# Optimization experiments

Measured on AMD Instinct MI355X. Metric: run time of the kernel, lower is better.

## Reference

```python
import jax, jax.numpy as jnp
import numpy as np

B, L, F, H = 4096, 32, 28, 512  # batch, max CDR length (=input_size), features, hidden


def setup_inputs() -> dict:
    key = jax.random.key(0)
    ks = jax.random.split(key, 8)
    return {
        "input": jax.random.normal(ks[0], (B, L, F), jnp.float32),
        "unpacked_masks": jnp.ones((B, L, 1), jnp.float32),
        "bias_mat": jnp.zeros((B, L, F), jnp.float32),
        "conv1_w": jax.random.normal(ks[1], (F, F, 3), jnp.float32) * 0.1,
        "conv1_b": jnp.zeros((F,), jnp.float32),
        "conv_w": jax.random.normal(ks[2], (1, L, 1), jnp.float32) * 0.1,
        "conv_b": jnp.zeros((1,), jnp.float32),
        "fc1_w": jax.random.normal(ks[3], (1, H), jnp.float32) * 0.05,
        "fc1_b": jnp.zeros((1,), jnp.float32),
        "W_ih": jax.random.normal(ks[4], (4 * H, L), jnp.float32) * 0.1,
        "W_hh": jax.random.normal(ks[5], (4 * H, H), jnp.float32) * 0.05,
        "b_ih": jnp.zeros((4 * H,), jnp.float32),
        "b_hh": jnp.zeros((4 * H,), jnp.float32),
        "conv2_w": jax.random.normal(ks[6], (1, H, 1), jnp.float32) * 0.05,
        "conv2_b": jnp.zeros((1,), jnp.float32),
    }


def reference(input, unpacked_masks, bias_mat, conv1_w, conv1_b, conv_w, conv_b,
              fc1_w, fc1_b, W_ih, W_hh, b_ih, b_hh, conv2_w, conv2_b):
    b, l, f = input.shape
    h_dim = W_hh.shape[1]
    # --- conv1 residual block (eval mode: dropouts are identity) ---
    x_t = jnp.transpose(input, (0, 2, 1))  # [B, F, L]
    y = jax.lax.conv_general_dilated(
        x_t, conv1_w, window_strides=(1,), padding=[(1, 1)],
        dimension_numbers=("NCH", "OIH", "NCH")) + conv1_b[None, :, None]
    x = jnp.transpose(y, (0, 2, 1)) * unpacked_masks  # [B, L, F]
    x = jax.nn.elu(x) + input
    # --- u_a = Conv1d(L,1,1) over the length axis: [B, 1, F] (kept as [B, F]) ---
    u_a = jnp.einsum("blf,l->bf", x, conv_w[0, :, 0]) + conv_b  # [B, F]
    x_transposed = jnp.transpose(x, (0, 2, 1))  # [B, F, L]

    h0 = jnp.zeros((l, h_dim), input.dtype)
    c0 = jnp.zeros((l, h_dim), input.dtype)

    def step(carry, inps):
        h, c = carry
        u_b, xT_b, bias_b = inps  # [F], [F, L], [L, F]
        w_a = h @ fc1_w.T + fc1_b  # [L, 1]
        scores = jax.nn.leaky_relu(u_b[None, :] + w_a, 0.01) + bias_b  # [L, F]
        attn = jax.nn.softmax(scores, axis=0)  # softmax over dim 1 of [B, L, F]
        ctx = attn @ xT_b  # [L, F] @ [F, L] -> [L, L]
        gates = ctx @ W_ih.T + b_ih + h @ W_hh.T + b_hh  # [L, 4H]
        i_g, f_g, g_g, o_g = jnp.split(gates, 4, axis=-1)
        c_new = jax.nn.sigmoid(f_g) * c + jax.nn.sigmoid(i_g) * jnp.tanh(g_g)
        h_new = jax.nn.sigmoid(o_g) * jnp.tanh(c_new)
        return (h_new, c_new), h_new

    # The original loops over the batch dim, carrying (h, c) across iterations.
    (_, _), all_hidden = jax.lax.scan(step, (h0, c0), (u_a, x_transposed, bias_mat))
    # all_hidden: [B, L, H]
    out = jnp.einsum("blh,h->bl", all_hidden, conv2_w[0, :, 0])[..., None] + conv2_b  # [B, L, 1]
    return out * unpacked_masks
```

## Files before the change

kernel.cpp:

```cpp
#include <hip/hip_runtime.h>
#include <math.h>

#define NBATCH 4096
#define LSEQ   32
#define FDIM   28
#define HDIM   512
#define GBLK   64
#define HSTRIDE 548
#define XSTR    36

typedef int   i32x4 __attribute__((ext_vector_type(4)));
typedef float f32x4 __attribute__((ext_vector_type(4)));
typedef short short8 __attribute__((ext_vector_type(8)));

#define OFF_X    0u
#define OFF_UA   (OFF_X  + 4096u*896u)
#define OFF_BG   (OFF_UA + 4096u*28u)
#define OFF_H    (OFF_BG + 2048u)
#define OFF_BAR  (OFF_H  + 2u*32u*512u)
#define OFF_WFH  (OFF_BAR + 64u)
#define OFF_WFL  (OFF_WFH + 557056u)

__device__ __forceinline__ unsigned bfr(float x) {
    unsigned u = __builtin_bit_cast(unsigned, x);
    return (u + 0x7FFFu + ((u >> 16) & 1u)) >> 16;
}
__device__ __forceinline__ float fb(unsigned b) { return __builtin_bit_cast(float, b << 16); }
__device__ __forceinline__ unsigned packhl(float v) {
    unsigned h = bfr(v);
    unsigned l = bfr(v - fb(h));
    return h | (l << 16);
}
__device__ __forceinline__ float up(unsigned u) {
    return __builtin_bit_cast(float, u << 16) + __builtin_bit_cast(float, u & 0xFFFF0000u);
}
__device__ __forceinline__ float sigm(float v) { return 1.0f / (1.0f + __expf(-v)); }

__global__ __launch_bounds__(256) void prep_kernel(
    const float* __restrict__ input, const float* __restrict__ masks,
    const float* __restrict__ c1w, const float* __restrict__ c1b,
    const float* __restrict__ convw, const float* __restrict__ convb,
    float* __restrict__ xout, float* __restrict__ uaout)
{
    __shared__ float in_lds[32][28];
    __shared__ float w_lds[28][28][3];
    __shared__ float xo[32][28];
    __shared__ float m_lds[32];
    __shared__ float cb_lds[28];
    const int b = blockIdx.x, tid = threadIdx.x;

    for (int i = tid; i < 896; i += 256) in_lds[i / 28][i % 28] = input[(size_t)b * 896 + i];
    for (int i = tid; i < 2352; i += 256) {
        int o = i / 84, r = i % 84;
        w_lds[o][r / 3][r % 3] = c1w[i];
    }
    if (tid < 32) m_lds[tid] = masks[b * 32 + tid];
    if (tid < 28) cb_lds[tid] = c1b[tid];
    __syncthreads();

    for (int i = tid; i < 896; i += 256) {
        const int l = i / 28, f = i % 28;
        float acc = cb_lds[f];
        for (int ii = 0; ii < 28; ++ii) {
            if (l > 0)  acc = fmaf(in_lds[l - 1][ii], w_lds[f][ii][0], acc);
            acc = fmaf(in_lds[l][ii], w_lds[f][ii][1], acc);
            if (l < 31) acc = fmaf(in_lds[l + 1][ii], w_lds[f][ii][2], acc);
        }
        float v = acc * m_lds[l];
        v = (v > 0.f) ? v : expm1f(v);
        v += in_lds[l][f];
        xo[l][f] = v;
        xout[(size_t)b * 896 + i] = v;
    }
    __syncthreads();
    if (tid < 28) {
        float s = convb[0];
        for (int l = 0; l < 32; ++l) s = fmaf(xo[l][tid], convw[l], s);
        uaout[b * 28 + tid] = s;
    }
}

__global__ __launch_bounds__(256) void prepw_kernel(
    const float* __restrict__ bih, const float* __restrict__ bhh, float* __restrict__ BG)
{
    const int g = blockIdx.x * 256 + threadIdx.x;
    BG[g] = bih[g] + bhh[g];
}

__global__ __launch_bounds__(256) void prepf_kernel(
    const float* __restrict__ Wih, const float* __restrict__ Whh,
    unsigned* __restrict__ wfh, unsigned* __restrict__ wfl)
{
    const int id = blockIdx.x * 256 + threadIdx.x;
    const int lane = id & 63;
    int rest = id >> 6;
    const int ct = rest & 1; rest >>= 1;
    const int t = rest % 17, blk = rest / 17;
    const int n = lane & 15, kg = lane >> 4;
    const int c = ct * 16 + n;
    const int g = (c >> 3) * 512 + blk * 8 + (c & 7);
    const int kbase = t * 32 + kg * 8;
    i32x4 hv, lv;
    #pragma unroll
    for (int d = 0; d < 4; ++d) {
        const int k = kbase + 2 * d;
        float w0 = (k     < 512) ? Whh[(size_t)g * 512 + k]     : Wih[g * 32 + (k - 512)];
        float w1 = (k + 1 < 512) ? Whh[(size_t)g * 512 + k + 1] : Wih[g * 32 + (k + 1 - 512)];
        unsigned h0 = bfr(w0), h1 = bfr(w1);
        unsigned l0 = bfr(w0 - fb(h0)), l1 = bfr(w1 - fb(h1));
        ((unsigned*)&hv)[d] = h0 | (h1 << 16);
        ((unsigned*)&lv)[d] = l0 | (l1 << 16);
    }
    ((i32x4*)wfh)[id] = hv;
    ((i32x4*)wfl)[id] = lv;
}

__device__ __forceinline__ void stage_h16(const unsigned* hsrc, unsigned* h_lds, int tid)
{
    const int half = tid >> 7, t128 = tid & 127;
    const unsigned* p = hsrc + half * 8192 + t128 * 4;
    i32x4 v0, v1, v2, v3, v4, v5, v6, v7, v8, v9, v10, v11, v12, v13, v14, v15;
    asm volatile(
        "global_load_dwordx4 %0, %16, off sc0 sc1\n\t"
        "global_load_dwordx4 %1, %16, off offset:2048 sc0 sc1\n\t"
        "global_load_dwordx4 %2, %17, off sc0 sc1\n\t"
        "global_load_dwordx4 %3, %17, off offset:2048 sc0 sc1\n\t"
        "global_load_dwordx4 %4, %18, off sc0 sc1\n\t"
        "global_load_dwordx4 %5, %18, off offset:2048 sc0 sc1\n\t"
        "global_load_dwordx4 %6, %19, off sc0 sc1\n\t"
        "global_load_dwordx4 %7, %19, off offset:2048 sc0 sc1\n\t"
        "global_load_dwordx4 %8, %20, off sc0 sc1\n\t"
        "global_load_dwordx4 %9, %20, off offset:2048 sc0 sc1\n\t"
        "global_load_dwordx4 %10, %21, off sc0 sc1\n\t"
        "global_load_dwordx4 %11, %21, off offset:2048 sc0 sc1\n\t"
        "global_load_dwordx4 %12, %22, off sc0 sc1\n\t"
        "global_load_dwordx4 %13, %22, off offset:2048 sc0 sc1\n\t"
        "global_load_dwordx4 %14, %23, off sc0 sc1\n\t"
        "global_load_dwordx4 %15, %23, off offset:2048 sc0 sc1\n\t"
        "s_waitcnt vmcnt(0)"
        : "=&v"(v0), "=&v"(v1), "=&v"(v2), "=&v"(v3),
          "=&v"(v4), "=&v"(v5), "=&v"(v6), "=&v"(v7),
          "=&v"(v8), "=&v"(v9), "=&v"(v10), "=&v"(v11),
          "=&v"(v12), "=&v"(v13), "=&v"(v14), "=&v"(v15)
        : "v"(p), "v"(p + 1024), "v"(p + 2048), "v"(p + 3072),
          "v"(p + 4096), "v"(p + 5120), "v"(p + 6144), "v"(p + 7168)
        : "memory");
    const int col = t128 * 4;
    const int rb = half * 16;
    *(i32x4*)&h_lds[(rb +  0) * HSTRIDE + col] = v0;
    *(i32x4*)&h_lds[(rb +  1) * HSTRIDE + col] = v1;
    *(i32x4*)&h_lds[(rb +  2) * HSTRIDE + col] = v2;
    *(i32x4*)&h_lds[(rb +  3) * HSTRIDE + col] = v3;
    *(i32x4*)&h_lds[(rb +  4) * HSTRIDE + col] = v4;
    *(i32x4*)&h_lds[(rb +  5) * HSTRIDE + col] = v5;
    *(i32x4*)&h_lds[(rb +  6) * HSTRIDE + col] = v6;
    *(i32x4*)&h_lds[(rb +  7) * HSTRIDE + col] = v7;
    *(i32x4*)&h_lds[(rb +  8) * HSTRIDE + col] = v8;
    *(i32x4*)&h_lds[(rb +  9) * HSTRIDE + col] = v9;
    *(i32x4*)&h_lds[(rb + 10) * HSTRIDE + col] = v10;
    *(i32x4*)&h_lds[(rb + 11) * HSTRIDE + col] = v11;
    *(i32x4*)&h_lds[(rb + 12) * HSTRIDE + col] = v12;
    *(i32x4*)&h_lds[(rb + 13) * HSTRIDE + col] = v13;
    *(i32x4*)&h_lds[(rb + 14) * HSTRIDE + col] = v14;
    *(i32x4*)&h_lds[(rb + 15) * HSTRIDE + col] = v15;
}

__device__ __forceinline__ void build_frag(const unsigned* base, short8& hi, short8& lo)
{
    i32x4 ua = *(const i32x4*)base;
    i32x4 ub = *(const i32x4*)(base + 4);
    i32x4 h, l;
    h.x = (int)__builtin_amdgcn_perm((unsigned)ua.y, (unsigned)ua.x, 0x05040100u);
    l.x = (int)__builtin_amdgcn_perm((unsigned)ua.y, (unsigned)ua.x, 0x07060302u);
    h.y = (int)__builtin_amdgcn_perm((unsigned)ua.w, (unsigned)ua.z, 0x05040100u);
    l.y = (int)__builtin_amdgcn_perm((unsigned)ua.w, (unsigned)ua.z, 0x07060302u);
    h.z = (int)__builtin_amdgcn_perm((unsigned)ub.y, (unsigned)ub.x, 0x05040100u);
    l.z = (int)__builtin_amdgcn_perm((unsigned)ub.y, (unsigned)ub.x, 0x07060302u);
    h.w = (int)__builtin_amdgcn_perm((unsigned)ub.w, (unsigned)ub.z, 0x05040100u);
    l.w = (int)__builtin_amdgcn_perm((unsigned)ub.w, (unsigned)ub.z, 0x07060302u);
    hi = __builtin_bit_cast(short8, h);
    lo = __builtin_bit_cast(short8, l);
}

__device__ __forceinline__ float exact_gate(const unsigned* hrow,
    const float* __restrict__ Whh, const float* __restrict__ Wih, int g)
{
    const f32x4* wr = (const f32x4*)(Whh + (size_t)g * 512);
    float s = 0.f;
    #pragma unroll 4
    for (int q = 0; q < 128; ++q) {
        f32x4 w = wr[q];
        s += up(hrow[4 * q + 0]) * w.x + up(hrow[4 * q + 1]) * w.y
           + up(hrow[4 * q + 2]) * w.z + up(hrow[4 * q + 3]) * w.w;
    }
    const float* wi = Wih + g * 32;
    #pragma unroll 8
    for (int j = 0; j < 32; ++j) s += up(hrow[512 + j]) * wi[j];
    return s;
}

__device__ __forceinline__ void out_proj(const unsigned* h_lds, const float* c2w_lds, float c2b,
                                         const float* masks, float* out, int bb,
                                         int slot16, int seg16)
{
    float p0 = 0.f, p1 = 0.f;
    #pragma unroll
    for (int jj = 0; jj < 8; ++jj) {
        const int off = seg16 * 4 + 64 * jj;
        f32x4 w = *(const f32x4*)&c2w_lds[off];
        i32x4 h0 = *(const i32x4*)&h_lds[slot16 * HSTRIDE + off];
        i32x4 h1 = *(const i32x4*)&h_lds[(slot16 + 16) * HSTRIDE + off];
        p0 += up((unsigned)h0.x) * w.x + up((unsigned)h0.y) * w.y
            + up((unsigned)h0.z) * w.z + up((unsigned)h0.w) * w.w;
        p1 += up((unsigned)h1.x) * w.x + up((unsigned)h1.y) * w.y
            + up((unsigned)h1.z) * w.z + up((unsigned)h1.w) * w.w;
    }
    p0 += __shfl_xor(p0, 1); p0 += __shfl_xor(p0, 2);
    p0 += __shfl_xor(p0, 4); p0 += __shfl_xor(p0, 8);
    p1 += __shfl_xor(p1, 1); p1 += __shfl_xor(p1, 2);
    p1 += __shfl_xor(p1, 4); p1 += __shfl_xor(p1, 8);
    if (seg16 == 0) {
        out[bb * 32 + slot16]      = (p0 + c2b) * masks[bb * 32 + slot16];
        out[bb * 32 + slot16 + 16] = (p1 + c2b) * masks[bb * 32 + slot16 + 16];
    }
}

__global__ __launch_bounds__(256, 1) void rnn_serial(
    const float* __restrict__ xbuf, const float* __restrict__ uabuf,
    const float* __restrict__ BG,
    const unsigned* __restrict__ wfh, const unsigned* __restrict__ wfl,
    const float* __restrict__ Whh, const float* __restrict__ Wih,
    unsigned* hbuf, int* bar,
    const float* __restrict__ bias_mat, const float* __restrict__ masks,
    const float* __restrict__ fc1w, const float* __restrict__ fc1bp,
    const float* __restrict__ c2w, const float* __restrict__ c2bp,
    float* __restrict__ out)
{
    __shared__ unsigned h_lds[32 * HSTRIDE];
    __shared__ float x_lds[32 * XSTR];
    __shared__ float bias_lds[32 * XSTR];
    __shared__ float attn_lds[32 * XSTR];
    __shared__ float gl_part[4 * 32 * 33];
    __shared__ float wapart[4][2][32];
    __shared__ float wa_lds[32];
    __shared__ float ua_lds[28];
    __shared__ float fc1_lds[512];
    __shared__ float c2w_lds[512];
    __shared__ int   s_flag;

    const int tid  = threadIdx.x;
    const int blk  = blockIdx.x;
    const int lane = tid & 63;
    const int wv   = tid >> 6;

    for (int i = tid; i < 512; i += 256) { fc1_lds[i] = fc1w[i]; c2w_lds[i] = c2w[i]; }
    if (tid == 0) s_flag = 0;
    const float f1b = fc1bp[0];
    const float c2b = c2bp[0];

    i32x4 whi[4][2], wlo[4][2];
    {
        const i32x4* wfh4 = (const i32x4*)wfh;
        const i32x4* wfl4 = (const i32x4*)wfl;
        #pragma unroll
        for (int s = 0; s < 4; ++s)
            #pragma unroll
            for (int ct = 0; ct < 2; ++ct) {
                const int idx = ((blk * 17 + wv * 4 + s) * 2 + ct) * 64 + lane;
                whi[s][ct] = wfh4[idx];
                wlo[s][ct] = wfl4[idx];
            }
    }
    i32x4 w16h[2], w16l[2];
    if (wv == 0) {
        const i32x4* wfh4 = (const i32x4*)wfh;
        const i32x4* wfl4 = (const i32x4*)wfl;
        #pragma unroll
        for (int ct = 0; ct < 2; ++ct) {
            const int idx = ((blk * 17 + 16) * 2 + ct) * 64 + lane;
            w16h[ct] = wfh4[idx];
            w16l[ct] = wfl4[idx];
        }
    }
    i32x4 wAh[4], wAl[4];
    {
        const int n = lane & 15, kg = lane >> 4;
        #pragma unroll
        for (int s = 0; s < 4; ++s) {
            wAh[s] = (i32x4){0, 0, 0, 0};
            wAl[s] = (i32x4){0, 0, 0, 0};
            if (n < 2) {
                const float* src = (n == 0) ? fc1w : c2w;
                const int k0 = (wv * 4 + s) * 32 + kg * 8;
                #pragma unroll
                for (int d = 0; d < 4; ++d) {
                    float v0 = src[k0 + 2 * d], v1 = src[k0 + 2 * d + 1];
                    unsigned h0 = bfr(v0), h1 = bfr(v1);
                    unsigned l0 = bfr(v0 - fb(h0)), l1 = bfr(v1 - fb(h1));
                    ((unsigned*)&wAh[s])[d] = h0 | (h1 << 16);
                    ((unsigned*)&wAl[s])[d] = l0 | (l1 << 16);
                }
            }
        }
    }

    const int l_own = tid >> 3, hc = tid & 7;
    float bgv[4];
    #pragma unroll
    for (int t = 0; t < 4; ++t) bgv[t] = BG[t * 512 + blk * 8 + hc];
    float c_reg = 0.f;
    bool use_mfma = true;

    float4 xr = make_float4(0.f, 0.f, 0.f, 0.f), br = xr;
    float ua_r = 0.f;
    if (tid < 224) {
        xr = *(const float4*)(xbuf + tid * 4);
        br = *(const float4*)(bias_mat + tid * 4);
    }
    if (tid < 28) ua_r = uabuf[tid];

    const int slot16 = tid >> 4, seg16 = tid & 15;
    const int arow = lane & 15, kg = lane >> 4;
    __syncthreads();

    for (int b = 0; b < NBATCH; ++b) {
        stage_h16(hbuf + (b & 1) * 16384, h_lds, tid);
        if (tid < 224) {
            #pragma unroll
            for (int i = 0; i < 4; ++i) {
                const int idx = tid * 4 + i;
                const int l = idx / 28, f = idx - l * 28;
                x_lds[l * XSTR + f]    = ((const float*)&xr)[i];
                bias_lds[l * XSTR + f] = ((const float*)&br)[i];
            }
        }
        if (tid < 28) ua_lds[tid] = ua_r;
        __syncthreads();

        f32x4 accg[2][2], accw[2];
        if (use_mfma) {
            accg[0][0] = (f32x4){0,0,0,0}; accg[0][1] = (f32x4){0,0,0,0};
            accg[1][0] = (f32x4){0,0,0,0}; accg[1][1] = (f32x4){0,0,0,0};
            accw[0]    = (f32x4){0,0,0,0}; accw[1]    = (f32x4){0,0,0,0};
            #pragma unroll
            for (int s = 0; s < 4; ++s) {
                const int k0 = (wv * 4 + s) * 32 + kg * 8;
                short8 ah0, al0, ah1, al1;
                build_frag(&h_lds[arow * HSTRIDE + k0], ah0, al0);
                build_frag(&h_lds[(arow + 16) * HSTRIDE + k0], ah1, al1);
                #pragma unroll
                for (int ct = 0; ct < 2; ++ct) {
                    short8 bh = __builtin_bit_cast(short8, whi[s][ct]);
                    short8 bl = __builtin_bit_cast(short8, wlo[s][ct]);
                    accg[ct][0] = __builtin_amdgcn_mfma_f32_16x16x32_bf16(ah0, bh, accg[ct][0], 0, 0, 0);
                    accg[ct][0] = __builtin_amdgcn_mfma_f32_16x16x32_bf16(al0, bh, accg[ct][0], 0, 0, 0);
                    accg[ct][0] = __builtin_amdgcn_mfma_f32_16x16x32_bf16(ah0, bl, accg[ct][0], 0, 0, 0);
                    accg[ct][1] = __builtin_amdgcn_mfma_f32_16x16x32_bf16(ah1, bh, accg[ct][1], 0, 0, 0);
                    accg[ct][1] = __builtin_amdgcn_mfma_f32_16x16x32_bf16(al1, bh, accg[ct][1], 0, 0, 0);
                    accg[ct][1] = __builtin_amdgcn_mfma_f32_16x16x32_bf16(ah1, bl, accg[ct][1], 0, 0, 0);
                }
                short8 bh = __builtin_bit_cast(short8, wAh[s]);
                short8 bl = __builtin_bit_cast(short8, wAl[s]);
                accw[0] = __builtin_amdgcn_mfma_f32_16x16x32_bf16(ah0, bh, accw[0], 0, 0, 0);
                accw[0] = __builtin_amdgcn_mfma_f32_16x16x32_bf16(al0, bh, accw[0], 0, 0, 0);
                accw[0] = __builtin_amdgcn_mfma_f32_16x16x32_bf16(ah0, bl, accw[0], 0, 0, 0);
                accw[1] = __builtin_amdgcn_mfma_f32_16x16x32_bf16(ah1, bh, accw[1], 0, 0, 0);
                accw[1] = __builtin_amdgcn_mfma_f32_16x16x32_bf16(al1, bh, accw[1], 0, 0, 0);
                accw[1] = __builtin_amdgcn_mfma_f32_16x16x32_bf16(ah1, bl, accw[1], 0, 0, 0);
            }
            if (wv != 0) {
                #pragma unroll
                for (int ct = 0; ct < 2; ++ct)
                    #pragma unroll
                    for (int rt = 0; rt < 2; ++rt)
                        #pragma unroll
                        for (int r = 0; r < 4; ++r)
                            gl_part[(wv * 32 + rt * 16 + kg * 4 + r) * 33 + ct * 16 + (lane & 15)] = accg[ct][rt][r];
            }
            const int n = lane & 15;
            if (n < 2) {
                #pragma unroll
                for (int rt = 0; rt < 2; ++rt)
                    #pragma unroll
                    for (int r = 0; r < 4; ++r)
                        wapart[wv][n][rt * 16 + kg * 4 + r] = accw[rt][r];
            }
        }
        if (b < 2 || !use_mfma) {
            float p0 = 0.f, p1 = 0.f;
            #pragma unroll
            for (int jj = 0; jj < 8; ++jj) {
                const int off = seg16 * 4 + 64 * jj;
                f32x4 w = *(const f32x4*)&fc1_lds[off];
                i32x4 h0 = *(const i32x4*)&h_lds[slot16 * HSTRIDE + off];
                i32x4 h1 = *(const i32x4*)&h_lds[(slot16 + 16) * HSTRIDE + off];
                p0 += up((unsigned)h0.x) * w.x + up((unsigned)h0.y) * w.y
                    + up((unsigned)h0.z) * w.z + up((unsigned)h0.w) * w.w;
                p1 += up((unsigned)h1.x) * w.x + up((unsigned)h1.y) * w.y
                    + up((unsigned)h1.z) * w.z + up((unsigned)h1.w) * w.w;
            }
            p0 += __shfl_xor(p0, 1); p0 += __shfl_xor(p0, 2);
            p0 += __shfl_xor(p0, 4); p0 += __shfl_xor(p0, 8);
            p1 += __shfl_xor(p1, 1); p1 += __shfl_xor(p1, 2);
            p1 += __shfl_xor(p1, 4); p1 += __shfl_xor(p1, 8);
            if (seg16 == 0) { wa_lds[slot16] = p0 + f1b; wa_lds[slot16 + 16] = p1 + f1b; }
            if (b > 0 && blk == ((b - 1) & 63))
                out_proj(h_lds, c2w_lds, c2b, masks, out, b - 1, slot16, seg16);
        }
        __syncthreads();

        if (wv == 3) {
            if (use_mfma && lane < 32) {
                float wm = f1b;
                #pragma unroll
                for (int w = 0; w < 4; ++w) wm += wapart[w][0][lane];
                if (b < 2) {
                    if (fabsf(wm - wa_lds[lane]) > 0.02f + 0.004f * fabsf(wa_lds[lane])) s_flag = 1;
                } else {
                    wa_lds[lane] = wm;
                }
            }
            if (lane < 56) {
                const int f = lane >> 1, hf = lane & 1;
                const float uaf = ua_lds[f];
                float z[16], mx = -1e30f;
                #pragma unroll
                for (int i = 0; i < 16; ++i) {
                    const int l = hf * 16 + i;
                    float v = uaf + wa_lds[l];
                    v = (v >= 0.f) ? v : 0.01f * v;
                    v += bias_lds[l * XSTR + f];
                    z[i] = v;
                    mx = fmaxf(mx, v);
                }
                mx = fmaxf(mx, __shfl_xor(mx, 1));
                float sum = 0.f;
                #pragma unroll
                for (int i = 0; i < 16; ++i) { z[i] = __expf(z[i] - mx); sum += z[i]; }
                sum += __shfl_xor(sum, 1);
                const float inv = 1.0f / sum;
                #pragma unroll
                for (int i = 0; i < 16; ++i) attn_lds[(hf * 16 + i) * XSTR + f] = z[i] * inv;
            }
        } else if (wv == 2 && use_mfma && lane < 32) {
            float om = c2b;
            #pragma unroll
            for (int w = 0; w < 4; ++w) om += wapart[w][1][lane];
            if (b < 2) {
                const unsigned* hr = &h_lds[lane * HSTRIDE];
                float ox = c2b;
                for (int k = 0; k < 512; ++k) ox += up(hr[k]) * c2w_lds[k];
                if (fabsf(om - ox) > 0.02f + 0.004f * fabsf(ox)) s_flag = 1;
            } else if (b > 0 && blk == ((b - 1) & 63)) {
                out[(b - 1) * 32 + lane] = om * masks[(b - 1) * 32 + lane];
            }
        }
        __syncthreads();

        {
            const int j0 = hc * 4;
            float t0v = 0.f, t1v = 0.f, t2v = 0.f, t3v = 0.f;
            #pragma unroll
            for (int fo = 0; fo < 7; ++fo) {
                f32x4 a4 = *(const f32x4*)&attn_lds[l_own * XSTR + fo * 4];
                f32x4 x0 = *(const f32x4*)&x_lds[(j0 + 0) * XSTR + fo * 4];
                f32x4 x1 = *(const f32x4*)&x_lds[(j0 + 1) * XSTR + fo * 4];
                f32x4 x2 = *(const f32x4*)&x_lds[(j0 + 2) * XSTR + fo * 4];
                f32x4 x3 = *(const f32x4*)&x_lds[(j0 + 3) * XSTR + fo * 4];
                t0v += a4.x * x0.x + a4.y * x0.y + a4.z * x0.z + a4.w * x0.w;
                t1v += a4.x * x1.x + a4.y * x1.y + a4.z * x1.z + a4.w * x1.w;
                t2v += a4.x * x2.x + a4.y * x2.y + a4.z * x2.z + a4.w * x2.w;
                t3v += a4.x * x3.x + a4.y * x3.y + a4.z * x3.z + a4.w * x3.w;
            }
            i32x4 cp;
            cp.x = (int)packhl(t0v); cp.y = (int)packhl(t1v);
            cp.z = (int)packhl(t2v); cp.w = (int)packhl(t3v);
            *(i32x4*)&h_lds[l_own * HSTRIDE + 512 + j0] = cp;
        }
        {
            const int bn = (b + 1 < NBATCH) ? b + 1 : 0;
            if (tid < 224) {
                xr = *(const float4*)(xbuf + (size_t)bn * 896 + tid * 4);
                br = *(const float4*)(bias_mat + (size_t)bn * 896 + tid * 4);
            }
            if (tid < 28) ua_r = uabuf[bn * 28 + tid];
        }
        __syncthreads();

        if (use_mfma && wv == 0) {
            short8 ah0, al0, ah1, al1;
            build_frag(&h_lds[arow * HSTRIDE + 512 + kg * 8], ah0, al0);
            build_frag(&h_lds[(arow + 16) * HSTRIDE + 512 + kg * 8], ah1, al1);
            #pragma unroll
            for (int ct = 0; ct < 2; ++ct) {
                short8 bh = __builtin_bit_cast(short8, w16h[ct]);
                short8 bl = __builtin_bit_cast(short8, w16l[ct]);
                accg[ct][0] = __builtin_amdgcn_mfma_f32_16x16x32_bf16(ah0, bh, accg[ct][0], 0, 0, 0);
                accg[ct][0] = __builtin_amdgcn_mfma_f32_16x16x32_bf16(al0, bh, accg[ct][0], 0, 0, 0);
                accg[ct][0] = __builtin_amdgcn_mfma_f32_16x16x32_bf16(ah0, bl, accg[ct][0], 0, 0, 0);
                accg[ct][1] = __builtin_amdgcn_mfma_f32_16x16x32_bf16(ah1, bh, accg[ct][1], 0, 0, 0);
                accg[ct][1] = __builtin_amdgcn_mfma_f32_16x16x32_bf16(al1, bh, accg[ct][1], 0, 0, 0);
                accg[ct][1] = __builtin_amdgcn_mfma_f32_16x16x32_bf16(ah1, bl, accg[ct][1], 0, 0, 0);
            }
            #pragma unroll
            for (int ct = 0; ct < 2; ++ct)
                #pragma unroll
                for (int rt = 0; rt < 2; ++rt)
                    #pragma unroll
                    for (int r = 0; r < 4; ++r)
                        gl_part[(rt * 16 + kg * 4 + r) * 33 + ct * 16 + (lane & 15)] = accg[ct][rt][r];
        }
        __syncthreads();

        {
            float gv[4];
            #pragma unroll
            for (int t = 0; t < 4; ++t) {
                float g = bgv[t];
                if (use_mfma) {
                    #pragma unroll
                    for (int w = 0; w < 4; ++w)
                        g += gl_part[(w * 32 + l_own) * 33 + t * 8 + hc];
                }
                gv[t] = g;
            }
            if (b < 2) {
                bool bad = false;
                #pragma unroll
                for (int t = 0; t < 4; ++t) {
                    float ref = bgv[t] + exact_gate(&h_lds[l_own * HSTRIDE], Whh, Wih,
                                                    t * 512 + blk * 8 + hc);
                    if (use_mfma && fabsf(gv[t] - ref) > 0.02f + 0.004f * fabsf(ref)) bad = true;
                    gv[t] = ref;
                }
                if (bad) s_flag = 1;
                __syncthreads();
                use_mfma = use_mfma && (s_flag == 0);
                __syncthreads();
                if (tid == 0) s_flag = 0;
            } else if (!use_mfma) {
                #pragma unroll
                for (int t = 0; t < 4; ++t)
                    gv[t] = bgv[t] + exact_gate(&h_lds[l_own * HSTRIDE], Whh, Wih,
                                                t * 512 + blk * 8 + hc);
            }
            const float cn = sigm(gv[1]) * c_reg + sigm(gv[0]) * tanhf(gv[2]);
            const float hn = sigm(gv[3]) * tanhf(cn);
            c_reg = cn;
            __hip_atomic_store(hbuf + ((b & 1) ^ 1) * 16384 + l_own * 512 + blk * 8 + hc,
                               packhl(hn), __ATOMIC_RELAXED, __HIP_MEMORY_SCOPE_AGENT);
        }
        asm volatile("s_waitcnt vmcnt(0)" ::: "memory");
        __syncthreads();
        if (tid == 0)
            __hip_atomic_store(&bar[blk], b + 1, __ATOMIC_RELAXED, __HIP_MEMORY_SCOPE_AGENT);
        if (tid < 64) {
            while (true) {
                int v = __hip_atomic_load(&bar[tid], __ATOMIC_RELAXED, __HIP_MEMORY_SCOPE_AGENT);
                if (__all(v >= b + 1)) break;
                __builtin_amdgcn_s_sleep(1);
            }
        }
        __syncthreads();
    }

    if (blk == 63) {
        stage_h16(hbuf, h_lds, tid);
        __syncthreads();
        if (use_mfma) {
            f32x4 accw[2];
            accw[0] = (f32x4){0,0,0,0}; accw[1] = (f32x4){0,0,0,0};
            #pragma unroll
            for (int s = 0; s < 4; ++s) {
                const int k0 = (wv * 4 + s) * 32 + kg * 8;
                short8 ah0, al0, ah1, al1;
                build_frag(&h_lds[arow * HSTRIDE + k0], ah0, al0);
                build_frag(&h_lds[(arow + 16) * HSTRIDE + k0], ah1, al1);
                short8 bh = __builtin_bit_cast(short8, wAh[s]);
                short8 bl = __builtin_bit_cast(short8, wAl[s]);
                accw[0] = __builtin_amdgcn_mfma_f32_16x16x32_bf16(ah0, bh, accw[0], 0, 0, 0);
                accw[0] = __builtin_amdgcn_mfma_f32_16x16x32_bf16(al0, bh, accw[0], 0, 0, 0);
                accw[0] = __builtin_amdgcn_mfma_f32_16x16x32_bf16(ah0, bl, accw[0], 0, 0, 0);
                accw[1] = __builtin_amdgcn_mfma_f32_16x16x32_bf16(ah1, bh, accw[1], 0, 0, 0);
                accw[1] = __builtin_amdgcn_mfma_f32_16x16x32_bf16(al1, bh, accw[1], 0, 0, 0);
                accw[1] = __builtin_amdgcn_mfma_f32_16x16x32_bf16(ah1, bl, accw[1], 0, 0, 0);
            }
            const int n = lane & 15;
            if (n < 2) {
                #pragma unroll
                for (int rt = 0; rt < 2; ++rt)
                    #pragma unroll
                    for (int r = 0; r < 4; ++r)
                        wapart[wv][n][rt * 16 + kg * 4 + r] = accw[rt][r];
            }
            __syncthreads();
            if (wv == 2 && lane < 32) {
                float om = c2b;
                #pragma unroll
                for (int w = 0; w < 4; ++w) om += wapart[w][1][lane];
                out[4095 * 32 + lane] = om * masks[4095 * 32 + lane];
            }
        } else {
            out_proj(h_lds, c2w_lds, c2b, masks, out, 4095, slot16, seg16);
        }
    }
}

extern "C" void kernel_launch(void* const* d_in, const int* in_sizes, int n_in,
                              void* d_out, int out_size, void* d_ws, size_t ws_size,
                              hipStream_t stream)
{
    const float* input    = (const float*)d_in[0];
    const float* masks    = (const float*)d_in[1];
    const float* bias_mat = (const float*)d_in[2];
    const float* c1w      = (const float*)d_in[3];
    const float* c1b      = (const float*)d_in[4];
    const float* convw    = (const float*)d_in[5];
    const float* convb    = (const float*)d_in[6];
    const float* fc1w     = (const float*)d_in[7];
    const float* fc1b     = (const float*)d_in[8];
    const float* Wih      = (const float*)d_in[9];
    const float* Whh      = (const float*)d_in[10];
    const float* bih      = (const float*)d_in[11];
    const float* bhh      = (const float*)d_in[12];
    const float* c2w      = (const float*)d_in[13];
    const float* c2b      = (const float*)d_in[14];

    float* ws  = (float*)d_ws;
    float* out = (float*)d_out;
    int*   bar = (int*)(ws + OFF_BAR);

    hipMemsetAsync(ws + OFF_H, 0, (2u * 32u * 512u + 64u) * sizeof(float), stream);

    hipLaunchKernelGGL(prep_kernel, dim3(NBATCH), dim3(256), 0, stream,
                       input, masks, c1w, c1b, convw, convb, ws + OFF_X, ws + OFF_UA);
    hipLaunchKernelGGL(prepw_kernel, dim3(8), dim3(256), 0, stream,
                       bih, bhh, ws + OFF_BG);
    hipLaunchKernelGGL(prepf_kernel, dim3(544), dim3(256), 0, stream,
                       Wih, Whh, (unsigned*)(ws + OFF_WFH), (unsigned*)(ws + OFF_WFL));
    hipLaunchKernelGGL(rnn_serial, dim3(GBLK), dim3(256), 0, stream,
                       ws + OFF_X, ws + OFF_UA, ws + OFF_BG,
                       (const unsigned*)(ws + OFF_WFH), (const unsigned*)(ws + OFF_WFL),
                       Whh, Wih,
                       (unsigned*)(ws + OFF_H), bar,
                       bias_mat, masks, fc1w, fc1b, c2w, c2b, out);
}
```

Baseline: 28.92 ms.

## Halve persistent grid to 32 blocks, each owning 16 hidden columns

The persistent serial LSTM kernel now runs on 32 workgroups instead of 64, and each one computes two 8-column hidden slices with twice the MFMA tiles per wave. The aim is to make the per-timestep grid barrier cheaper, since fewer blocks have to signal and be polled. In exchange each block does twice the gate math per step, holds more register-resident weights, and reloads the tail weight tile from global memory every step instead of keeping it in registers. This lengthens the critical path of each serial step.

```diff
diff --git a/kernel.cpp b/kernel.cpp
--- a/kernel.cpp
+++ b/kernel.cpp
@@ -2,12 +2,9 @@
 #include <math.h>
 
 #define NBATCH 4096
-#define LSEQ   32
-#define FDIM   28
-#define HDIM   512
-#define GBLK   64
+#define GBLK   32
 #define HSTRIDE 548
-#define XSTR    36
+#define XSTR   36
 
 typedef int   i32x4 __attribute__((ext_vector_type(4)));
 typedef float f32x4 __attribute__((ext_vector_type(4)));
@@ -95,10 +92,10 @@
     const int lane = id & 63;
     int rest = id >> 6;
     const int ct = rest & 1; rest >>= 1;
-    const int t = rest % 17, blk = rest / 17;
+    const int t = rest % 17, blk8 = rest / 17;
     const int n = lane & 15, kg = lane >> 4;
     const int c = ct * 16 + n;
-    const int g = (c >> 3) * 512 + blk * 8 + (c & 7);
+    const int g = (c >> 3) * 512 + blk8 * 8 + (c & 7);
     const int kbase = t * 32 + kg * 8;
     i32x4 hv, lv;
     #pragma unroll
@@ -240,7 +237,7 @@
     __shared__ float x_lds[32 * XSTR];
     __shared__ float bias_lds[32 * XSTR];
     __shared__ float attn_lds[32 * XSTR];
-    __shared__ float gl_part[4 * 32 * 33];
+    __shared__ float gl_part[5 * 32 * 65];
     __shared__ float wapart[4][2][32];
     __shared__ float wa_lds[32];
     __shared__ float ua_lds[28];
@@ -249,7 +246,7 @@
     __shared__ int   s_flag;
 
     const int tid  = threadIdx.x;
-    const int blk  = blockIdx.x;
+    const int rank = blockIdx.x;
     const int lane = tid & 63;
     const int wv   = tid >> 6;
 
@@ -258,40 +255,30 @@
     const float f1b = fc1bp[0];
     const float c2b = c2bp[0];
 
-    i32x4 whi[4][2], wlo[4][2];
+    i32x4 whi[4][4], wlo[4][4];
     {
         const i32x4* wfh4 = (const i32x4*)wfh;
         const i32x4* wfl4 = (const i32x4*)wfl;
         #pragma unroll
         for (int s = 0; s < 4; ++s)
             #pragma unroll
-            for (int ct = 0; ct < 2; ++ct) {
-                const int idx = ((blk * 17 + wv * 4 + s) * 2 + ct) * 64 + lane;
+            for (int ct = 0; ct < 4; ++ct) {
+                const int blkOld = 2 * rank + (ct >> 1);
+                const int idx = ((blkOld * 17 + wv * 4 + s) * 2 + (ct & 1)) * 64 + lane;
                 whi[s][ct] = wfh4[idx];
                 wlo[s][ct] = wfl4[idx];
             }
     }
-    i32x4 w16h[2], w16l[2];
-    if (wv == 0) {
-        const i32x4* wfh4 = (const i32x4*)wfh;
-        const i32x4* wfl4 = (const i32x4*)wfl;
-        #pragma unroll
-        for (int ct = 0; ct < 2; ++ct) {
-            const int idx = ((blk * 17 + 16) * 2 + ct) * 64 + lane;
-            w16h[ct] = wfh4[idx];
-            w16l[ct] = wfl4[idx];
-        }
-    }
     i32x4 wAh[4], wAl[4];
     {
-        const int n = lane & 15, kg = lane >> 4;
+        const int n = lane & 15, kgi = lane >> 4;
         #pragma unroll
         for (int s = 0; s < 4; ++s) {
             wAh[s] = (i32x4){0, 0, 0, 0};
             wAl[s] = (i32x4){0, 0, 0, 0};
             if (n < 2) {
                 const float* src = (n == 0) ? fc1w : c2w;
-                const int k0 = (wv * 4 + s) * 32 + kg * 8;
+                const int k0 = (wv * 4 + s) * 32 + kgi * 8;
                 #pragma unroll
                 for (int d = 0; d < 4; ++d) {
                     float v0 = src[k0 + 2 * d], v1 = src[k0 + 2 * d + 1];
@@ -305,10 +292,13 @@
     }
 
     const int l_own = tid >> 3, hc = tid & 7;
-    float bgv[4];
+    float bgv[2][4];
     #pragma unroll
-    for (int t = 0; t < 4; ++t) bgv[t] = BG[t * 512 + blk * 8 + hc];
-    float c_reg = 0.f;
+    for (int j = 0; j < 2; ++j)
+        #pragma unroll
+        for (int t = 0; t < 4; ++t)
+            bgv[j][t] = BG[t * 512 + rank * 16 + hc + 8 * j];
+    float creg[2] = {0.f, 0.f};
     bool use_mfma = true;
 
     float4 xr = make_float4(0.f, 0.f, 0.f, 0.f), br = xr;
@@ -337,11 +327,14 @@
         if (tid < 28) ua_lds[tid] = ua_r;
         __syncthreads();
 
-        f32x4 accg[2][2], accw[2];
         if (use_mfma) {
-            accg[0][0] = (f32x4){0,0,0,0}; accg[0][1] = (f32x4){0,0,0,0};
-            accg[1][0] = (f32x4){0,0,0,0}; accg[1][1] = (f32x4){0,0,0,0};
-            accw[0]    = (f32x4){0,0,0,0}; accw[1]    = (f32x4){0,0,0,0};
+            f32x4 accg[4][2], accw[2];
+            #pragma unroll
+            for (int ct = 0; ct < 4; ++ct) {
+                accg[ct][0] = (f32x4){0,0,0,0};
+                accg[ct][1] = (f32x4){0,0,0,0};
+            }
+            accw[0] = (f32x4){0,0,0,0}; accw[1] = (f32x4){0,0,0,0};
             #pragma unroll
             for (int s = 0; s < 4; ++s) {
                 const int k0 = (wv * 4 + s) * 32 + kg * 8;
@@ -349,7 +342,7 @@
                 build_frag(&h_lds[arow * HSTRIDE + k0], ah0, al0);
                 build_frag(&h_lds[(arow + 16) * HSTRIDE + k0], ah1, al1);
                 #pragma unroll
-                for (int ct = 0; ct < 2; ++ct) {
+                for (int ct = 0; ct < 4; ++ct) {
                     short8 bh = __builtin_bit_cast(short8, whi[s][ct]);
                     short8 bl = __builtin_bit_cast(short8, wlo[s][ct]);
                     accg[ct][0] = __builtin_amdgcn_mfma_f32_16x16x32_bf16(ah0, bh, accg[ct][0], 0, 0, 0);
@@ -368,22 +361,19 @@
                 accw[1] = __builtin_amdgcn_mfma_f32_16x16x32_bf16(al1, bh, accw[1], 0, 0, 0);
                 accw[1] = __builtin_amdgcn_mfma_f32_16x16x32_bf16(ah1, bl, accw[1], 0, 0, 0);
             }
-            if (wv != 0) {
-                #pragma unroll
-                for (int ct = 0; ct < 2; ++ct)
-                    #pragma unroll
-                    for (int rt = 0; rt < 2; ++rt)
-                        #pragma unroll
-                        for (int r = 0; r < 4; ++r)
-                            gl_part[(wv * 32 + rt * 16 + kg * 4 + r) * 33 + ct * 16 + (lane & 15)] = accg[ct][rt][r];
-            }
-            const int n = lane & 15;
-            if (n < 2) {
+            #pragma unroll
+            for (int ct = 0; ct < 4; ++ct)
                 #pragma unroll
                 for (int rt = 0; rt < 2; ++rt)
                     #pragma unroll
                     for (int r = 0; r < 4; ++r)
-                        wapart[wv][n][rt * 16 + kg * 4 + r] = accw[rt][r];
+                        gl_part[(wv * 32 + rt * 16 + kg * 4 + r) * 65 + ct * 16 + arow] = accg[ct][rt][r];
+            if (arow < 2) {
+                #pragma unroll
+                for (int rt = 0; rt < 2; ++rt)
+                    #pragma unroll
+                    for (int r = 0; r < 4; ++r)
+                        wapart[wv][arow][rt * 16 + kg * 4 + r] = accw[rt][r];
             }
         }
         if (b < 2 || !use_mfma) {
@@ -404,7 +394,7 @@
             p1 += __shfl_xor(p1, 1); p1 += __shfl_xor(p1, 2);
             p1 += __shfl_xor(p1, 4); p1 += __shfl_xor(p1, 8);
             if (seg16 == 0) { wa_lds[slot16] = p0 + f1b; wa_lds[slot16 + 16] = p1 + f1b; }
-            if (b > 0 && blk == ((b - 1) & 63))
+            if (b > 0 && rank == ((b - 1) & 31))
                 out_proj(h_lds, c2w_lds, c2b, masks, out, b - 1, slot16, seg16);
         }
         __syncthreads();
@@ -451,7 +441,7 @@
                 float ox = c2b;
                 for (int k = 0; k < 512; ++k) ox += up(hr[k]) * c2w_lds[k];
                 if (fabsf(om - ox) > 0.02f + 0.004f * fabsf(ox)) s_flag = 1;
-            } else if (b > 0 && blk == ((b - 1) & 63)) {
+            } else if (b > 0 && rank == ((b - 1) & 31)) {
                 out[(b - 1) * 32 + lane] = om * masks[(b - 1) * 32 + lane];
             }
         }
@@ -487,52 +477,60 @@
         }
         __syncthreads();
 
-        if (use_mfma && wv == 0) {
+        if (use_mfma && wv < 2) {
             short8 ah0, al0, ah1, al1;
             build_frag(&h_lds[arow * HSTRIDE + 512 + kg * 8], ah0, al0);
             build_frag(&h_lds[(arow + 16) * HSTRIDE + 512 + kg * 8], ah1, al1);
-            #pragma unroll
-            for (int ct = 0; ct < 2; ++ct) {
-                short8 bh = __builtin_bit_cast(short8, w16h[ct]);
-                short8 bl = __builtin_bit_cast(short8, w16l[ct]);
-                accg[ct][0] = __builtin_amdgcn_mfma_f32_16x16x32_bf16(ah0, bh, accg[ct][0], 0, 0, 0);
-                accg[ct][0] = __builtin_amdgcn_mfma_f32_16x16x32_bf16(al0, bh, accg[ct][0], 0, 0, 0);
-                accg[ct][0] = __builtin_amdgcn_mfma_f32_16x16x32_bf16(ah0, bl, accg[ct][0], 0, 0, 0);
-                accg[ct][1] = __builtin_amdgcn_mfma_f32_16x16x32_bf16(ah1, bh, accg[ct][1], 0, 0, 0);
-                accg[ct][1] = __builtin_amdgcn_mfma_f32_16x16x32_bf16(al1, bh, accg[ct][1], 0, 0, 0);
-                accg[ct][1] = __builtin_amdgcn_mfma_f32_16x16x32_bf16(ah1, bl, accg[ct][1], 0, 0, 0);
-            }
-            #pragma unroll
-            for (int ct = 0; ct < 2; ++ct)
-                #pragma unroll
-                for (int rt = 0; rt < 2; ++rt)
-                    #pragma unroll
-                    for (int r = 0; r < 4; ++r)
-                        gl_part[(rt * 16 + kg * 4 + r) * 33 + ct * 16 + (lane & 15)] = accg[ct][rt][r];
+            const i32x4* wfh4 = (const i32x4*)wfh;
+            const i32x4* wfl4 = (const i32x4*)wfl;
+            #pragma unroll
+            for (int q = 0; q < 2; ++q) {
+                const int ct4 = wv * 2 + q;
+                const int idx = (((2 * rank + (ct4 >> 1)) * 17 + 16) * 2 + (ct4 & 1)) * 64 + lane;
+                short8 bh = __builtin_bit_cast(short8, wfh4[idx]);
+                short8 bl = __builtin_bit_cast(short8, wfl4[idx]);
+                f32x4 a0 = (f32x4){0,0,0,0}, a1 = (f32x4){0,0,0,0};
+                a0 = __builtin_amdgcn_mfma_f32_16x16x32_bf16(ah0, bh, a0, 0, 0, 0);
+                a0 = __builtin_amdgcn_mfma_f32_16x16x32_bf16(al0, bh, a0, 0, 0, 0);
+                a0 = __builtin_amdgcn_mfma_f32_16x16x32_bf16(ah0, bl, a0, 0, 0, 0);
+                a1 = __builtin_amdgcn_mfma_f32_16x16x32_bf16(ah1, bh, a1, 0, 0, 0);
+                a1 = __builtin_amdgcn_mfma_f32_16x16x32_bf16(al1, bh, a1, 0, 0, 0);
+                a1 = __builtin_amdgcn_mfma_f32_16x16x32_bf16(ah1, bl, a1, 0, 0, 0);
+                #pragma unroll
+                for (int r = 0; r < 4; ++r) {
+                    gl_part[(4 * 32 +      kg * 4 + r) * 65 + ct4 * 16 + arow] = a0[r];
+                    gl_part[(4 * 32 + 16 + kg * 4 + r) * 65 + ct4 * 16 + arow] = a1[r];
+                }
+            }
         }
         __syncthreads();
 
         {
-            float gv[4];
-            #pragma unroll
-            for (int t = 0; t < 4; ++t) {
-                float g = bgv[t];
-                if (use_mfma) {
-                    #pragma unroll
-                    for (int w = 0; w < 4; ++w)
-                        g += gl_part[(w * 32 + l_own) * 33 + t * 8 + hc];
+            float gv[2][4];
+            #pragma unroll
+            for (int j = 0; j < 2; ++j)
+                #pragma unroll
+                for (int t = 0; t < 4; ++t) {
+                    float g = bgv[j][t];
+                    if (use_mfma) {
+                        const int co = (j * 2 + ((t * 8 + hc) >> 4)) * 16 + ((t * 8 + hc) & 15);
+                        #pragma unroll
+                        for (int w = 0; w < 5; ++w)
+                            g += gl_part[(w * 32 + l_own) * 65 + co];
+                    }
+                    gv[j][t] = g;
                 }
-                gv[t] = g;
-            }
             if (b < 2) {
                 bool bad = false;
                 #pragma unroll
-                for (int t = 0; t < 4; ++t) {
-                    float ref = bgv[t] + exact_gate(&h_lds[l_own * HSTRIDE], Whh, Wih,
-                                                    t * 512 + blk * 8 + hc);
-                    if (use_mfma && fabsf(gv[t] - ref) > 0.02f + 0.004f * fabsf(ref)) bad = true;
-                    gv[t] = ref;
-                }
+                for (int j = 0; j < 2; ++j)
+                    #pragma unroll
+                    for (int t = 0; t < 4; ++t) {
+                        float ref = bgv[j][t] + exact_gate(&h_lds[l_own * HSTRIDE], Whh, Wih,
+                                                           t * 512 + rank * 16 + hc + 8 * j);
+                        if (use_mfma && fabsf(gv[j][t] - ref) > 0.02f + 0.004f * fabsf(ref)) bad = true;
+                        gv[j][t] = ref;
+                    }
                 if (bad) s_flag = 1;
                 __syncthreads();
                 use_mfma = use_mfma && (s_flag == 0);
@@ -540,23 +538,30 @@
                 if (tid == 0) s_flag = 0;
             } else if (!use_mfma) {
                 #pragma unroll
-                for (int t = 0; t < 4; ++t)
-                    gv[t] = bgv[t] + exact_gate(&h_lds[l_own * HSTRIDE], Whh, Wih,
-                                                t * 512 + blk * 8 + hc);
-            }
-            const float cn = sigm(gv[1]) * c_reg + sigm(gv[0]) * tanhf(gv[2]);
-            const float hn = sigm(gv[3]) * tanhf(cn);
-            c_reg = cn;
-            __hip_atomic_store(hbuf + ((b & 1) ^ 1) * 16384 + l_own * 512 + blk * 8 + hc,
-                               packhl(hn), __ATOMIC_RELAXED, __HIP_MEMORY_SCOPE_AGENT);
-        }
+                for (int j = 0; j < 2; ++j)
+                    #pragma unroll
+                    for (int t = 0; t < 4; ++t)
+                        gv[j][t] = bgv[j][t] + exact_gate(&h_lds[l_own * HSTRIDE], Whh, Wih,
+                                                          t * 512 + rank * 16 + hc + 8 * j);
+            }
+            unsigned* hdst = hbuf + ((b & 1) ^ 1) * 16384 + l_own * 512 + rank * 16 + hc;
+            #pragma unroll
+            for (int j = 0; j < 2; ++j) {
+                const float cn = sigm(gv[j][1]) * creg[j] + sigm(gv[j][0]) * tanhf(gv[j][2]);
+                const float hn = sigm(gv[j][3]) * tanhf(cn);
+                creg[j] = cn;
+                __hip_atomic_store(hdst + 8 * j, packhl(hn),
+                                   __ATOMIC_RELAXED, __HIP_MEMORY_SCOPE_AGENT);
+            }
+        }
+
         asm volatile("s_waitcnt vmcnt(0)" ::: "memory");
         __syncthreads();
         if (tid == 0)
-            __hip_atomic_store(&bar[blk], b + 1, __ATOMIC_RELAXED, __HIP_MEMORY_SCOPE_AGENT);
+            __hip_atomic_store(&bar[rank], b + 1, __ATOMIC_RELAXED, __HIP_MEMORY_SCOPE_AGENT);
         if (tid < 64) {
             while (true) {
-                int v = __hip_atomic_load(&bar[tid], __ATOMIC_RELAXED, __HIP_MEMORY_SCOPE_AGENT);
+                int v = __hip_atomic_load(&bar[tid & 31], __ATOMIC_RELAXED, __HIP_MEMORY_SCOPE_AGENT);
                 if (__all(v >= b + 1)) break;
                 __builtin_amdgcn_s_sleep(1);
             }
@@ -564,7 +569,7 @@
         __syncthreads();
     }
 
-    if (blk == 63) {
+    if (rank == 31) {
         stage_h16(hbuf, h_lds, tid);
         __syncthreads();
         if (use_mfma) {
@@ -585,13 +590,12 @@
                 accw[1] = __builtin_amdgcn_mfma_f32_16x16x32_bf16(al1, bh, accw[1], 0, 0, 0);
                 accw[1] = __builtin_amdgcn_mfma_f32_16x16x32_bf16(ah1, bl, accw[1], 0, 0, 0);
             }
-            const int n = lane & 15;
-            if (n < 2) {
+            if (arow < 2) {
                 #pragma unroll
                 for (int rt = 0; rt < 2; ++rt)
                     #pragma unroll
                     for (int r = 0; r < 4; ++r)
-                        wapart[wv][n][rt * 16 + kg * 4 + r] = accw[rt][r];
+                        wapart[wv][arow][rt * 16 + kg * 4 + r] = accw[rt][r];
             }
             __syncthreads();
             if (wv == 2 && lane < 32) {
```

New measurement: 30.98 ms. 7.1% more time.
